# Kernel optimization log

Measured on AMD Instinct MI355X. Metric: run time of the kernel, lower is better.

The kernel has to match this reference:

```python
import jax, jax.numpy as jnp
import numpy as np

FT_IN = 49152   # HalfKA feature space
VFT_IN = 768    # virtual (factored) feature space
FT_OUT = 512
BATCH = 8192
MAX_FEATS = 32  # max active features (pieces) per position
NNZ = BATCH * MAX_FEATS


def setup_inputs() -> dict:
    key = jax.random.key(0)
    ks = jax.random.split(key, 9)
    bidx = jnp.repeat(jnp.arange(BATCH, dtype=jnp.int64), MAX_FEATS)
    stm_feat = jax.random.randint(ks[0], (NNZ,), 0, FT_IN, dtype=jnp.int64)
    nstm_feat = jax.random.randint(ks[1], (NNZ,), 0, FT_IN, dtype=jnp.int64)
    stm_indices = jnp.stack([bidx, stm_feat])    # [2, nnz]
    nstm_indices = jnp.stack([bidx, nstm_feat])  # [2, nnz]
    values = jnp.ones((NNZ,), dtype=jnp.float32)
    s = 1.0 / np.sqrt(FT_IN)
    sv = 1.0 / np.sqrt(VFT_IN)
    so = 1.0 / np.sqrt(2 * FT_OUT)
    return {
        "stm_indices": stm_indices,
        "nstm_indices": nstm_indices,
        "values": values,
        "size": BATCH,
        "W_ft": jax.random.uniform(ks[2], (FT_IN, FT_OUT), jnp.float32, -s, s),
        "b_ft": jax.random.uniform(ks[3], (FT_OUT,), jnp.float32, -s, s),
        "W_fft": jax.random.uniform(ks[4], (VFT_IN, FT_OUT), jnp.float32, -sv, sv),
        "b_fft": jax.random.uniform(ks[5], (VFT_IN if False else FT_OUT,), jnp.float32, -sv, sv),
        "W_out": jax.random.uniform(ks[6], (2 * FT_OUT, 1), jnp.float32, -so, so),
        "b_out": jax.random.uniform(ks[7], (1,), jnp.float32, -so, so),
    }


def _perspective_ft(indices, values, size, W_ft, b_ft, W_fft, b_fft):
    # sparse feature-transformer: sum over active features of
    # (W_ft[f] + W_fft[f % 768]) * value, per batch row.
    bidx = indices[0]
    feat = indices[1]
    rows = values[:, None] * (W_ft[feat] + W_fft[feat % VFT_IN])  # [nnz, ft_out]
    acc = jax.ops.segment_sum(rows, bidx, num_segments=size)       # [B, ft_out]
    return acc + b_ft + b_fft


def reference(stm_indices, nstm_indices, values, size,
              W_ft, b_ft, W_fft, b_fft, W_out, b_out):
    stm_ft = _perspective_ft(stm_indices, values, size, W_ft, b_ft, W_fft, b_fft)
    nstm_ft = _perspective_ft(nstm_indices, values, size, W_ft, b_ft, W_fft, b_fft)
    hidden = jnp.clip(jnp.concatenate([stm_ft, nstm_ft], axis=1), 0.0, 1.0)
    return jax.nn.sigmoid(hidden @ W_out + b_out)  # [B, 1]
```

## Files before the change

### kernel.cpp

```cpp
#include <hip/hip_runtime.h>
#include <math.h>

#define MAXF   32
#define FTOUT  512
#define VFT    768
#define FTIN   49152
#define NCHUNK 8
#define CCOLS  64
#define RPB    32

__global__ __launch_bounds__(256)
void build_wsum(const float* __restrict__ W_ft,
                const float* __restrict__ W_fft,
                unsigned short* __restrict__ Wsum)
{
    const long long e = ((long long)blockIdx.x * blockDim.x + threadIdx.x) * 4;
    const int f = (int)(e >> 9);
    const int j = (int)(e & 511);
    const float4 a = *(const float4*)(W_ft + e);
    const float4 c = *(const float4*)(W_fft + (long long)(f % VFT) * FTOUT + j);
    const float s[4] = {a.x + c.x, a.y + c.y, a.z + c.z, a.w + c.w};
    ushort4 o;
    unsigned short* op = (unsigned short*)&o;
    #pragma unroll
    for (int t = 0; t < 4; ++t) {
        unsigned int u = __float_as_uint(s[t]);
        u += 0x7FFFu + ((u >> 16) & 1u);
        op[t] = (unsigned short)(u >> 16);
    }
    *(ushort4*)(Wsum + e) = o;
}

__global__ __launch_bounds__(256)
void prep_idx(const int* __restrict__ stm_idx,
              const int* __restrict__ nstm_idx,
              const float* __restrict__ values,
              int* __restrict__ off32,
              float* __restrict__ val32,
              int nnz, int batch)
{
    const int t = blockIdx.x * 256 + threadIdx.x;
    if (t >= batch * 64) return;
    const int b = t >> 6;
    const int k = t & 63;
    const int g = b * MAXF + (k & 31);
    const int f = (k < 32 ? stm_idx : nstm_idx)[nnz + g];
    off32[t] = f * FTOUT;
    if (k < 32) val32[b * 32 + k] = values[g];
}

#define CONS(A, W, V) do {                                        \
    A[0] = fmaf(V, __uint_as_float((W).x << 16),         A[0]);   \
    A[1] = fmaf(V, __uint_as_float((W).x & 0xFFFF0000u), A[1]);   \
    A[2] = fmaf(V, __uint_as_float((W).y << 16),         A[2]);   \
    A[3] = fmaf(V, __uint_as_float((W).y & 0xFFFF0000u), A[3]);   \
    A[4] = fmaf(V, __uint_as_float((W).z << 16),         A[4]);   \
    A[5] = fmaf(V, __uint_as_float((W).z & 0xFFFF0000u), A[5]);   \
    A[6] = fmaf(V, __uint_as_float((W).w << 16),         A[6]);   \
    A[7] = fmaf(V, __uint_as_float((W).w & 0xFFFF0000u), A[7]);   \
} while (0)

__global__ __launch_bounds__(256, 4)
void gather_chunk(const unsigned short* __restrict__ Wsum,
                  const int* __restrict__ off32,
                  const float* __restrict__ val32,
                  const float* __restrict__ b_ft,
                  const float* __restrict__ b_fft,
                  const float* __restrict__ W_out,
                  float* __restrict__ partial,
                  int batch)
{
    const int c    = blockIdx.x & (NCHUNK - 1);
    const int rg   = blockIdx.x >> 3;
    const int tid  = threadIdx.x;
    const int wid  = tid >> 6;
    const int lane = tid & 63;
    const int lg   = lane >> 3;
    const int cg   = lane & 7;
    const int col0 = c * CCOLS + cg * 8;

    float bb[8], wos[8], won[8];
    {
        const float4 a0 = *(const float4*)(b_ft + col0);
        const float4 a1 = *(const float4*)(b_ft + col0 + 4);
        const float4 f0 = *(const float4*)(b_fft + col0);
        const float4 f1 = *(const float4*)(b_fft + col0 + 4);
        bb[0]=a0.x+f0.x; bb[1]=a0.y+f0.y; bb[2]=a0.z+f0.z; bb[3]=a0.w+f0.w;
        bb[4]=a1.x+f1.x; bb[5]=a1.y+f1.y; bb[6]=a1.z+f1.z; bb[7]=a1.w+f1.w;
        const float4 s0 = *(const float4*)(W_out + col0);
        const float4 s1 = *(const float4*)(W_out + col0 + 4);
        const float4 n0 = *(const float4*)(W_out + FTOUT + col0);
        const float4 n1 = *(const float4*)(W_out + FTOUT + col0 + 4);
        wos[0]=s0.x; wos[1]=s0.y; wos[2]=s0.z; wos[3]=s0.w;
        wos[4]=s1.x; wos[5]=s1.y; wos[6]=s1.z; wos[7]=s1.w;
        won[0]=n0.x; won[1]=n0.y; won[2]=n0.z; won[3]=n0.w;
        won[4]=n1.x; won[5]=n1.y; won[6]=n1.z; won[7]=n1.w;
    }
    const unsigned short* base = Wsum + col0;
    const int row0 = rg * RPB + wid * 8;

    for (int r = 0; r < 8; ++r) {
        const int row = row0 + r;
        if (row >= batch) break;

        const int   off_all = off32[row * 64 + lane];
        const float v_all   = val32[row * 32 + (lane & 31)];

        const int o0 = __shfl(off_all,      lg);
        const int o1 = __shfl(off_all,  8 + lg);
        const int o2 = __shfl(off_all, 16 + lg);
        const int o3 = __shfl(off_all, 24 + lg);
        const int o4 = __shfl(off_all, 32 + lg);
        const int o5 = __shfl(off_all, 40 + lg);
        const int o6 = __shfl(off_all, 48 + lg);
        const int o7 = __shfl(off_all, 56 + lg);

        const uint4 w0 = *(const uint4*)(base + o0);
        const uint4 w1 = *(const uint4*)(base + o1);
        const uint4 w2 = *(const uint4*)(base + o2);
        const uint4 w3 = *(const uint4*)(base + o3);
        const uint4 w4 = *(const uint4*)(base + o4);
        const uint4 w5 = *(const uint4*)(base + o5);
        const uint4 w6 = *(const uint4*)(base + o6);
        const uint4 w7 = *(const uint4*)(base + o7);
        __builtin_amdgcn_sched_barrier(0);

        const float v0 = __shfl(v_all,      lg);
        const float v1 = __shfl(v_all,  8 + lg);
        const float v2 = __shfl(v_all, 16 + lg);
        const float v3 = __shfl(v_all, 24 + lg);

        float acc_s[8] = {0.f,0.f,0.f,0.f,0.f,0.f,0.f,0.f};
        float acc_n[8] = {0.f,0.f,0.f,0.f,0.f,0.f,0.f,0.f};
        CONS(acc_s, w0, v0); CONS(acc_s, w1, v1);
        CONS(acc_s, w2, v2); CONS(acc_s, w3, v3);
        CONS(acc_n, w4, v0); CONS(acc_n, w5, v1);
        CONS(acc_n, w6, v2); CONS(acc_n, w7, v3);

        #pragma unroll
        for (int t = 0; t < 8; ++t) {
            acc_s[t] += __shfl_xor(acc_s[t], 8);
            acc_n[t] += __shfl_xor(acc_n[t], 8);
        }
        #pragma unroll
        for (int t = 0; t < 8; ++t) {
            acc_s[t] += __shfl_xor(acc_s[t], 16);
            acc_n[t] += __shfl_xor(acc_n[t], 16);
        }
        #pragma unroll
        for (int t = 0; t < 8; ++t) {
            acc_s[t] += __shfl_xor(acc_s[t], 32);
            acc_n[t] += __shfl_xor(acc_n[t], 32);
        }

        float part = 0.f;
        #pragma unroll
        for (int t = 0; t < 8; ++t) {
            const float hs = fminf(fmaxf(acc_s[t] + bb[t], 0.f), 1.f);
            part = fmaf(hs, wos[t], part);
        }
        #pragma unroll
        for (int t = 0; t < 8; ++t) {
            const float hn = fminf(fmaxf(acc_n[t] + bb[t], 0.f), 1.f);
            part = fmaf(hn, won[t], part);
        }
        part += __shfl_xor(part, 1);
        part += __shfl_xor(part, 2);
        part += __shfl_xor(part, 4);

        if (lane == 0) partial[row * NCHUNK + c] = part;
    }
}

__global__ __launch_bounds__(256)
void final_out(const float* __restrict__ partial,
               const float* __restrict__ b_out,
               float* __restrict__ out, int batch)
{
    const int b = blockIdx.x * 256 + threadIdx.x;
    if (b >= batch) return;
    const float4 p0 = *(const float4*)(partial + b * NCHUNK);
    const float4 p1 = *(const float4*)(partial + b * NCHUNK + 4);
    const float tot = ((p0.x + p0.y) + (p0.z + p0.w))
                    + ((p1.x + p1.y) + (p1.z + p1.w)) + b_out[0];
    out[b] = 1.0f / (1.0f + expf(-tot));
}

__global__ __launch_bounds__(128, 8)
void nnhalfka_gather(const int* __restrict__ stm_idx,
                     const int* __restrict__ nstm_idx,
                     const float* __restrict__ values,
                     const unsigned short* __restrict__ Wsum,
                     const float* __restrict__ b_ft,
                     const float* __restrict__ b_fft,
                     const float* __restrict__ W_out,
                     const float* __restrict__ b_out,
                     float* __restrict__ out,
                     int nnz)
{
    const int b    = blockIdx.x;
    const int tid  = threadIdx.x;
    const int wave = tid >> 6;
    const int lane = tid & 63;

    __shared__ int   s_off[2][MAXF];
    __shared__ float s_v[MAXF];
    __shared__ float s_red[2];

    if (lane < MAXF) {
        const int g = b * MAXF + lane;
        const int* src = wave ? nstm_idx : stm_idx;
        s_off[wave][lane] = src[nnz + g] * FTOUT;
    } else if (wave == 0) {
        s_v[lane - MAXF] = values[b * MAXF + (lane - MAXF)];
    }
    __syncthreads();

    const int jbase = lane * 8;
    float acc[8] = {0.f,0.f,0.f,0.f,0.f,0.f,0.f,0.f};

    #pragma unroll
    for (int g8 = 0; g8 < MAXF / 8; ++g8) {
        uint4 q0 = *(const uint4*)(Wsum + s_off[wave][g8*8+0] + jbase);
        uint4 q1 = *(const uint4*)(Wsum + s_off[wave][g8*8+1] + jbase);
        uint4 q2 = *(const uint4*)(Wsum + s_off[wave][g8*8+2] + jbase);
        uint4 q3 = *(const uint4*)(Wsum + s_off[wave][g8*8+3] + jbase);
        uint4 q4 = *(const uint4*)(Wsum + s_off[wave][g8*8+4] + jbase);
        uint4 q5 = *(const uint4*)(Wsum + s_off[wave][g8*8+5] + jbase);
        uint4 q6 = *(const uint4*)(Wsum + s_off[wave][g8*8+6] + jbase);
        uint4 q7 = *(const uint4*)(Wsum + s_off[wave][g8*8+7] + jbase);
        __builtin_amdgcn_sched_barrier(0);
        CONS(acc, q0, s_v[g8*8+0]); CONS(acc, q1, s_v[g8*8+1]);
        CONS(acc, q2, s_v[g8*8+2]); CONS(acc, q3, s_v[g8*8+3]);
        CONS(acc, q4, s_v[g8*8+4]); CONS(acc, q5, s_v[g8*8+5]);
        CONS(acc, q6, s_v[g8*8+6]); CONS(acc, q7, s_v[g8*8+7]);
    }

    float bb[8], wo[8];
    *(float4*)&bb[0] = *(const float4*)(b_ft + jbase);
    *(float4*)&bb[4] = *(const float4*)(b_ft + jbase + 4);
    {
        const float4 v0 = *(const float4*)(b_fft + jbase);
        const float4 v1 = *(const float4*)(b_fft + jbase + 4);
        bb[0]+=v0.x; bb[1]+=v0.y; bb[2]+=v0.z; bb[3]+=v0.w;
        bb[4]+=v1.x; bb[5]+=v1.y; bb[6]+=v1.z; bb[7]+=v1.w;
    }
    *(float4*)&wo[0] = *(const float4*)(W_out + wave * FTOUT + jbase);
    *(float4*)&wo[4] = *(const float4*)(W_out + wave * FTOUT + jbase + 4);

    float partial = 0.f;
    #pragma unroll
    for (int t = 0; t < 8; ++t) {
        const float h = fminf(fmaxf(acc[t] + bb[t], 0.f), 1.f);
        partial = fmaf(h, wo[t], partial);
    }
    #pragma unroll
    for (int off = 32; off > 0; off >>= 1)
        partial += __shfl_down(partial, off);
    if (lane == 0) s_red[wave] = partial;
    __syncthreads();
    if (tid == 0) {
        const float tot = s_red[0] + s_red[1] + b_out[0];
        out[b] = 1.0f / (1.0f + expf(-tot));
    }
}

__global__ __launch_bounds__(256)
void nnhalfka_fused(const int* __restrict__ stm_idx,
                    const int* __restrict__ nstm_idx,
                    const float* __restrict__ values,
                    const float* __restrict__ W_ft,
                    const float* __restrict__ b_ft,
                    const float* __restrict__ W_fft,
                    const float* __restrict__ b_fft,
                    const float* __restrict__ W_out,
                    const float* __restrict__ b_out,
                    float* __restrict__ out,
                    int nnz)
{
    const int b   = blockIdx.x;
    const int tid = threadIdx.x;

    __shared__ int   s_fs[MAXF], s_fsm[MAXF], s_fn[MAXF], s_fnm[MAXF];
    __shared__ float s_v[MAXF];
    __shared__ float s_red[4];

    if (tid < MAXF) {
        const int g  = b * MAXF + tid;
        const int fs = stm_idx[nnz + g];
        const int fn = nstm_idx[nnz + g];
        s_fs[tid]  = fs * FTOUT;
        s_fsm[tid] = (fs % VFT) * FTOUT;
        s_fn[tid]  = fn * FTOUT;
        s_fnm[tid] = (fn % VFT) * FTOUT;
        s_v[tid]   = values[g];
    }
    __syncthreads();

    const int j = tid * 2;
    float2 accs = make_float2(0.f, 0.f);
    float2 accn = make_float2(0.f, 0.f);

    #pragma unroll 4
    for (int k = 0; k < MAXF; ++k) {
        const float v    = s_v[k];
        const float2 ws  = *(const float2*)(W_ft  + s_fs[k]  + j);
        const float2 wfs = *(const float2*)(W_fft + s_fsm[k] + j);
        const float2 wn  = *(const float2*)(W_ft  + s_fn[k]  + j);
        const float2 wfn = *(const float2*)(W_fft + s_fnm[k] + j);
        accs.x += v * (ws.x + wfs.x);
        accs.y += v * (ws.y + wfs.y);
        accn.x += v * (wn.x + wfn.x);
        accn.y += v * (wn.y + wfn.y);
    }

    const float bb0 = b_ft[j]     + b_fft[j];
    const float bb1 = b_ft[j + 1] + b_fft[j + 1];
    const float hs0 = fminf(fmaxf(accs.x + bb0, 0.f), 1.f);
    const float hs1 = fminf(fmaxf(accs.y + bb1, 0.f), 1.f);
    const float hn0 = fminf(fmaxf(accn.x + bb0, 0.f), 1.f);
    const float hn1 = fminf(fmaxf(accn.y + bb1, 0.f), 1.f);

    float partial = hs0 * W_out[j]         + hs1 * W_out[j + 1]
                  + hn0 * W_out[FTOUT + j] + hn1 * W_out[FTOUT + j + 1];
    #pragma unroll
    for (int off = 32; off > 0; off >>= 1)
        partial += __shfl_down(partial, off);
    if ((tid & 63) == 0) s_red[tid >> 6] = partial;
    __syncthreads();
    if (tid == 0) {
        const float tot = s_red[0] + s_red[1] + s_red[2] + s_red[3] + b_out[0];
        out[b] = 1.0f / (1.0f + expf(-tot));
    }
}

extern "C" void kernel_launch(void* const* d_in, const int* in_sizes, int n_in,
                              void* d_out, int out_size, void* d_ws, size_t ws_size,
                              hipStream_t stream) {
    const int*   stm_idx  = (const int*)d_in[0];
    const int*   nstm_idx = (const int*)d_in[1];
    const float* values   = (const float*)d_in[2];
    const float* W_ft     = (const float*)d_in[4];
    const float* b_ft     = (const float*)d_in[5];
    const float* W_fft    = (const float*)d_in[6];
    const float* b_fft    = (const float*)d_in[7];
    const float* W_out    = (const float*)d_in[8];
    const float* b_out    = (const float*)d_in[9];
    float* out = (float*)d_out;

    const int nnz   = in_sizes[0] / 2;
    const int batch = out_size;

    const size_t WSUM_B = (size_t)FTIN * FTOUT * 2;
    const size_t OFF_B  = (size_t)batch * 64 * 4;
    const size_t VAL_B  = (size_t)batch * 32 * 4;
    const size_t PART_B = (size_t)batch * NCHUNK * 4;
    const size_t need_chunked = WSUM_B + OFF_B + VAL_B + PART_B;

    if (ws_size >= need_chunked) {
        unsigned short* Wsum = (unsigned short*)d_ws;
        int*   off32   = (int*)((char*)d_ws + WSUM_B);
        float* val32   = (float*)((char*)d_ws + WSUM_B + OFF_B);
        float* partial = (float*)((char*)d_ws + WSUM_B + OFF_B + VAL_B);

        build_wsum<<<(FTIN * FTOUT / 4) / 256, 256, 0, stream>>>(W_ft, W_fft, Wsum);
        prep_idx<<<(batch * 64 + 255) / 256, 256, 0, stream>>>(
            stm_idx, nstm_idx, values, off32, val32, nnz, batch);
        gather_chunk<<<((batch + RPB - 1) / RPB) * NCHUNK, 256, 0, stream>>>(
            Wsum, off32, val32, b_ft, b_fft, W_out, partial, batch);
        final_out<<<(batch + 255) / 256, 256, 0, stream>>>(partial, b_out, out, batch);
    } else if (ws_size >= WSUM_B) {
        unsigned short* Wsum = (unsigned short*)d_ws;
        build_wsum<<<(FTIN * FTOUT / 4) / 256, 256, 0, stream>>>(W_ft, W_fft, Wsum);
        nnhalfka_gather<<<batch, 128, 0, stream>>>(
            stm_idx, nstm_idx, values, Wsum, b_ft, b_fft, W_out, b_out, out, nnz);
    } else {
        nnhalfka_fused<<<batch, 256, 0, stream>>>(
            stm_idx, nstm_idx, values, W_ft, b_ft, W_fft, b_fft, W_out, b_out,
            out, nnz);
    }
}
```

Before: 83.83 us.

## Stage per-row offsets in LDS and split wave into two rows per iteration

The gather kernel now loads the 32 rows' feature byte offsets and values into shared memory once per block instead of reading and shuffling them per row. Each wave handles two rows at a time (half-wave per row) with four feature groups of eight loads each, which removes one xor-reduction stage and issues 16 gathers per thread per row. The bias is folded into the accumulator init, pre-divided by four so the four-way reduction restores it. This trades extra LDS use and a block barrier for fewer shuffles and more memory-level parallelism per thread.

```diff
diff --git a/kernel.cpp b/kernel.cpp
--- a/kernel.cpp
+++ b/kernel.cpp
@@ -6,7 +6,6 @@
 #define VFT    768
 #define FTIN   49152
 #define NCHUNK 8
-#define CCOLS  64
 #define RPB    32
 
 __global__ __launch_bounds__(256)
@@ -45,7 +44,7 @@
     const int k = t & 63;
     const int g = b * MAXF + (k & 31);
     const int f = (k < 32 ? stm_idx : nstm_idx)[nnz + g];
-    off32[t] = f * FTOUT;
+    off32[t] = f * (FTOUT * 2);
     if (k < 32) val32[b * 32 + k] = values[g];
 }
 
@@ -61,81 +60,115 @@
 } while (0)
 
 __global__ __launch_bounds__(256, 4)
-void gather_chunk(const unsigned short* __restrict__ Wsum,
-                  const int* __restrict__ off32,
-                  const float* __restrict__ val32,
-                  const float* __restrict__ b_ft,
-                  const float* __restrict__ b_fft,
-                  const float* __restrict__ W_out,
-                  float* __restrict__ partial,
-                  int batch)
+void gather_chunk2(const unsigned short* __restrict__ Wsum,
+                   const int* __restrict__ off32,
+                   const float* __restrict__ val32,
+                   const float* __restrict__ b_ft,
+                   const float* __restrict__ b_fft,
+                   const float* __restrict__ W_out,
+                   float* __restrict__ partial,
+                   int batch)
 {
     const int c    = blockIdx.x & (NCHUNK - 1);
     const int rg   = blockIdx.x >> 3;
     const int tid  = threadIdx.x;
     const int wid  = tid >> 6;
     const int lane = tid & 63;
-    const int lg   = lane >> 3;
+    const int r    = lane >> 5;
+    const int fg   = (lane >> 3) & 3;
     const int cg   = lane & 7;
-    const int col0 = c * CCOLS + cg * 8;
-
-    float bb[8], wos[8], won[8];
+
+    __shared__ int   s_off[RPB][64];
+    __shared__ float s_val[RPB][32];
+
+    const int row_base = rg * RPB;
+
+    #pragma unroll
+    for (int i = 0; i < 8; ++i) {
+        const int idx = i * 256 + tid;
+        const int gsrc = row_base * 64 + idx;
+        ((int*)s_off)[idx] = (gsrc < batch * 64) ? off32[gsrc] : 0;
+    }
+    #pragma unroll
+    for (int i = 0; i < 4; ++i) {
+        const int idx = i * 256 + tid;
+        const int gsrc = row_base * 32 + idx;
+        ((float*)s_val)[idx] = (gsrc < batch * 32) ? val32[gsrc] : 0.f;
+    }
+    __syncthreads();
+
+    const int col = c * 64 + cg * 8;
+    float bbq[8], wos[8], won[8];
     {
-        const float4 a0 = *(const float4*)(b_ft + col0);
-        const float4 a1 = *(const float4*)(b_ft + col0 + 4);
-        const float4 f0 = *(const float4*)(b_fft + col0);
-        const float4 f1 = *(const float4*)(b_fft + col0 + 4);
-        bb[0]=a0.x+f0.x; bb[1]=a0.y+f0.y; bb[2]=a0.z+f0.z; bb[3]=a0.w+f0.w;
-        bb[4]=a1.x+f1.x; bb[5]=a1.y+f1.y; bb[6]=a1.z+f1.z; bb[7]=a1.w+f1.w;
-        const float4 s0 = *(const float4*)(W_out + col0);
-        const float4 s1 = *(const float4*)(W_out + col0 + 4);
-        const float4 n0 = *(const float4*)(W_out + FTOUT + col0);
-        const float4 n1 = *(const float4*)(W_out + FTOUT + col0 + 4);
+        const float4 a0 = *(const float4*)(b_ft + col);
+        const float4 a1 = *(const float4*)(b_ft + col + 4);
+        const float4 f0 = *(const float4*)(b_fft + col);
+        const float4 f1 = *(const float4*)(b_fft + col + 4);
+        bbq[0]=(a0.x+f0.x)*0.25f; bbq[1]=(a0.y+f0.y)*0.25f;
+        bbq[2]=(a0.z+f0.z)*0.25f; bbq[3]=(a0.w+f0.w)*0.25f;
+        bbq[4]=(a1.x+f1.x)*0.25f; bbq[5]=(a1.y+f1.y)*0.25f;
+        bbq[6]=(a1.z+f1.z)*0.25f; bbq[7]=(a1.w+f1.w)*0.25f;
+        const float4 s0 = *(const float4*)(W_out + col);
+        const float4 s1 = *(const float4*)(W_out + col + 4);
+        const float4 n0 = *(const float4*)(W_out + FTOUT + col);
+        const float4 n1 = *(const float4*)(W_out + FTOUT + col + 4);
         wos[0]=s0.x; wos[1]=s0.y; wos[2]=s0.z; wos[3]=s0.w;
         wos[4]=s1.x; wos[5]=s1.y; wos[6]=s1.z; wos[7]=s1.w;
         won[0]=n0.x; won[1]=n0.y; won[2]=n0.z; won[3]=n0.w;
         won[4]=n1.x; won[5]=n1.y; won[6]=n1.z; won[7]=n1.w;
     }
-    const unsigned short* base = Wsum + col0;
-    const int row0 = rg * RPB + wid * 8;
-
-    for (int r = 0; r < 8; ++r) {
-        const int row = row0 + r;
-        if (row >= batch) break;
-
-        const int   off_all = off32[row * 64 + lane];
-        const float v_all   = val32[row * 32 + (lane & 31)];
-
-        const int o0 = __shfl(off_all,      lg);
-        const int o1 = __shfl(off_all,  8 + lg);
-        const int o2 = __shfl(off_all, 16 + lg);
-        const int o3 = __shfl(off_all, 24 + lg);
-        const int o4 = __shfl(off_all, 32 + lg);
-        const int o5 = __shfl(off_all, 40 + lg);
-        const int o6 = __shfl(off_all, 48 + lg);
-        const int o7 = __shfl(off_all, 56 + lg);
-
-        const uint4 w0 = *(const uint4*)(base + o0);
-        const uint4 w1 = *(const uint4*)(base + o1);
-        const uint4 w2 = *(const uint4*)(base + o2);
-        const uint4 w3 = *(const uint4*)(base + o3);
-        const uint4 w4 = *(const uint4*)(base + o4);
-        const uint4 w5 = *(const uint4*)(base + o5);
-        const uint4 w6 = *(const uint4*)(base + o6);
-        const uint4 w7 = *(const uint4*)(base + o7);
+
+    const char* wb = (const char*)Wsum;
+    const unsigned colb = (unsigned)(c * 128 + cg * 16);
+
+    #pragma unroll
+    for (int it = 0; it < 4; ++it) {
+        const int lrow  = wid * 8 + 2 * it + r;
+        const int row_g = row_base + lrow;
+
+        const int*   po = &s_off[lrow][fg];
+        const float* pv = &s_val[lrow][fg];
+
+        const int o0 = po[0],  o1 = po[4],  o2 = po[8],  o3 = po[12];
+        const int o4 = po[16], o5 = po[20], o6 = po[24], o7 = po[28];
+        const int q0 = po[32], q1 = po[36], q2 = po[40], q3 = po[44];
+        const int q4 = po[48], q5 = po[52], q6 = po[56], q7 = po[60];
+        const float v0 = pv[0],  v1 = pv[4],  v2 = pv[8],  v3 = pv[12];
+        const float v4 = pv[16], v5 = pv[20], v6 = pv[24], v7 = pv[28];
+
+        const uint4 a0 = *(const uint4*)(wb + (unsigned)o0 + colb);
+        const uint4 a1 = *(const uint4*)(wb + (unsigned)o1 + colb);
+        const uint4 a2 = *(const uint4*)(wb + (unsigned)o2 + colb);
+        const uint4 a3 = *(const uint4*)(wb + (unsigned)o3 + colb);
+        const uint4 a4 = *(const uint4*)(wb + (unsigned)o4 + colb);
+        const uint4 a5 = *(const uint4*)(wb + (unsigned)o5 + colb);
+        const uint4 a6 = *(const uint4*)(wb + (unsigned)o6 + colb);
+        const uint4 a7 = *(const uint4*)(wb + (unsigned)o7 + colb);
         __builtin_amdgcn_sched_barrier(0);
 
-        const float v0 = __shfl(v_all,      lg);
-        const float v1 = __shfl(v_all,  8 + lg);
-        const float v2 = __shfl(v_all, 16 + lg);
-        const float v3 = __shfl(v_all, 24 + lg);
-
-        float acc_s[8] = {0.f,0.f,0.f,0.f,0.f,0.f,0.f,0.f};
-        float acc_n[8] = {0.f,0.f,0.f,0.f,0.f,0.f,0.f,0.f};
-        CONS(acc_s, w0, v0); CONS(acc_s, w1, v1);
-        CONS(acc_s, w2, v2); CONS(acc_s, w3, v3);
-        CONS(acc_n, w4, v0); CONS(acc_n, w5, v1);
-        CONS(acc_n, w6, v2); CONS(acc_n, w7, v3);
+        float acc_s[8], acc_n[8];
+        #pragma unroll
+        for (int t = 0; t < 8; ++t) { acc_s[t] = bbq[t]; acc_n[t] = bbq[t]; }
+
+        CONS(acc_s, a0, v0); CONS(acc_s, a1, v1);
+        CONS(acc_s, a2, v2); CONS(acc_s, a3, v3);
+        CONS(acc_s, a4, v4); CONS(acc_s, a5, v5);
+        CONS(acc_s, a6, v6); CONS(acc_s, a7, v7);
+
+        const uint4 b0 = *(const uint4*)(wb + (unsigned)q0 + colb);
+        const uint4 b1 = *(const uint4*)(wb + (unsigned)q1 + colb);
+        const uint4 b2 = *(const uint4*)(wb + (unsigned)q2 + colb);
+        const uint4 b3 = *(const uint4*)(wb + (unsigned)q3 + colb);
+        const uint4 b4 = *(const uint4*)(wb + (unsigned)q4 + colb);
+        const uint4 b5 = *(const uint4*)(wb + (unsigned)q5 + colb);
+        const uint4 b6 = *(const uint4*)(wb + (unsigned)q6 + colb);
+        const uint4 b7 = *(const uint4*)(wb + (unsigned)q7 + colb);
+        __builtin_amdgcn_sched_barrier(0);
+
+        CONS(acc_n, b0, v0); CONS(acc_n, b1, v1);
+        CONS(acc_n, b2, v2); CONS(acc_n, b3, v3);
+        CONS(acc_n, b4, v4); CONS(acc_n, b5, v5);
+        CONS(acc_n, b6, v6); CONS(acc_n, b7, v7);
 
         #pragma unroll
         for (int t = 0; t < 8; ++t) {
@@ -147,28 +180,24 @@
             acc_s[t] += __shfl_xor(acc_s[t], 16);
             acc_n[t] += __shfl_xor(acc_n[t], 16);
         }
-        #pragma unroll
-        for (int t = 0; t < 8; ++t) {
-            acc_s[t] += __shfl_xor(acc_s[t], 32);
-            acc_n[t] += __shfl_xor(acc_n[t], 32);
-        }
 
         float part = 0.f;
         #pragma unroll
         for (int t = 0; t < 8; ++t) {
-            const float hs = fminf(fmaxf(acc_s[t] + bb[t], 0.f), 1.f);
+            const float hs = fminf(fmaxf(acc_s[t], 0.f), 1.f);
             part = fmaf(hs, wos[t], part);
         }
         #pragma unroll
         for (int t = 0; t < 8; ++t) {
-            const float hn = fminf(fmaxf(acc_n[t] + bb[t], 0.f), 1.f);
+            const float hn = fminf(fmaxf(acc_n[t], 0.f), 1.f);
             part = fmaf(hn, won[t], part);
         }
         part += __shfl_xor(part, 1);
         part += __shfl_xor(part, 2);
         part += __shfl_xor(part, 4);
 
-        if (lane == 0) partial[row * NCHUNK + c] = part;
+        if ((lane & 31) == 0 && row_g < batch)
+            partial[row_g * NCHUNK + c] = part;
     }
 }
 
@@ -366,7 +395,7 @@
         build_wsum<<<(FTIN * FTOUT / 4) / 256, 256, 0, stream>>>(W_ft, W_fft, Wsum);
         prep_idx<<<(batch * 64 + 255) / 256, 256, 0, stream>>>(
             stm_idx, nstm_idx, values, off32, val32, nnz, batch);
-        gather_chunk<<<((batch + RPB - 1) / RPB) * NCHUNK, 256, 0, stream>>>(
+        gather_chunk2<<<((batch + RPB - 1) / RPB) * NCHUNK, 256, 0, stream>>>(
             Wsum, off32, val32, b_ft, b_fft, W_out, partial, batch);
         final_out<<<(batch + 255) / 256, 256, 0, stream>>>(partial, b_out, out, batch);
     } else if (ws_size >= WSUM_B) {
```

New measurement: 80.00 us. -4.6%, faster.
